# Optimization experiments

Measured on AMD Instinct MI355X. Metric: run time of the kernel, lower is better.

## Reference

```python
import jax, jax.numpy as jnp
import numpy as np

MIN_NORM = 1e-15
C = 1.0  # ball curvature from init kwargs
N, D, O = 16384, 512, 512


def _expmap0(u, c):
    sqrt_c = c ** 0.5
    u_norm = jnp.maximum(jnp.linalg.norm(u, axis=-1, keepdims=True), MIN_NORM)
    return jnp.tanh(sqrt_c * u_norm) * u / (sqrt_c * u_norm)


def setup_inputs() -> dict:
    key = jax.random.key(0)
    k1, k2, k3 = jax.random.split(key, 3)
    # scale inputs so they lie inside the unit Poincare ball (E||x|| ~ 0.45)
    x = jax.random.normal(k1, (N, D), jnp.float32) * 0.02
    point = _expmap0(jax.random.normal(k2, (O, D), jnp.float32) / 4, C)
    tangent = jax.random.normal(k3, (O, D), jnp.float32)
    tangent = tangent / jnp.maximum(jnp.linalg.norm(tangent, axis=-1, keepdims=True), MIN_NORM)  # sphere proj_
    scale = jnp.zeros((O,), jnp.float32)
    return {"x": x, "point": point, "tangent": tangent, "scale": scale}


def reference(x, point, tangent, scale):
    """Mobius dist2plane (signed) * exp(scale).

    Computes the reductions of diff = mobius_add(-p, x) analytically so the
    [N, O, D] broadcast intermediate of the original is never materialized.
    """
    c = C
    sqrt_c = c ** 0.5
    p, a = point, tangent
    p2 = jnp.sum(p * p, -1)                 # [O]  ||p||^2
    x2 = jnp.sum(x * x, -1)                 # [N]  ||x||^2
    xp = x @ p.T                             # [N,O] <x, p>
    xy = -xp                                 # <-p, x>
    # mobius_add(-p, x) = (A*(-p) + B*x) / Dn
    A = 1 + 2 * c * xy + c * x2[:, None]     # [N,O] coeff of -p
    B = 1 - c * p2                           # [O]   coeff of x
    Dn = jnp.maximum(1 + 2 * c * xy + (c * c) * p2[None, :] * x2[:, None], MIN_NORM)  # [N,O]
    pa = jnp.sum(p * a, -1)                  # [O]  <p, a>
    xa = x @ a.T                             # [N,O] <x, a>
    diff_norm2 = (A * A * p2[None, :] - 2 * A * B[None, :] * xp
                  + (B * B)[None, :] * x2[:, None]) / (Dn * Dn)
    diff_norm2 = jnp.maximum(diff_norm2, MIN_NORM)
    sc_diff_a = (-A * pa[None, :] + B[None, :] * xa) / Dn  # <diff, a>
    a_norm = jnp.maximum(jnp.linalg.norm(a, axis=-1), MIN_NORM)  # [O]
    num = 2 * sqrt_c * sc_diff_a
    denom = jnp.maximum((1 - c * diff_norm2) * a_norm[None, :], MIN_NORM)
    dist = jnp.arcsinh(num / denom) / sqrt_c  # [N,O]
    return dist * jnp.exp(scale)
```

## Files before the change

kernel.cpp:

```cpp
#include <hip/hip_runtime.h>
#include <hip/hip_bf16.h>

typedef float f32x4 __attribute__((ext_vector_type(4)));
typedef short short8_t __attribute__((ext_vector_type(8)));

__device__ __forceinline__ unsigned int cvt2(float lo, float hi) {
    unsigned int ul = __builtin_bit_cast(unsigned int, lo);
    unsigned int uh = __builtin_bit_cast(unsigned int, hi);
    ul += 0x7FFFu + ((ul >> 16) & 1u);
    uh += 0x7FFFu + ((uh >> 16) & 1u);
    return (ul >> 16) | (uh & 0xFFFF0000u);
}

__device__ __forceinline__ float sq4(f32x4 v, float acc) {
    acc = fmaf(v[0], v[0], acc); acc = fmaf(v[1], v[1], acc);
    acc = fmaf(v[2], v[2], acc); acc = fmaf(v[3], v[3], acc);
    return acc;
}

__device__ __forceinline__ float dot4(f32x4 a, f32x4 b, float acc) {
    acc = fmaf(a[0], b[0], acc); acc = fmaf(a[1], b[1], acc);
    acc = fmaf(a[2], b[2], acc); acc = fmaf(a[3], b[3], acc);
    return acc;
}

__device__ __forceinline__ short8_t pk8(f32x4 a, f32x4 b) {
    union { short8_t s; unsigned int u[4]; } w;
    w.u[0] = cvt2(a[0], a[1]); w.u[1] = cvt2(a[2], a[3]);
    w.u[2] = cvt2(b[0], b[1]); w.u[3] = cvt2(b[2], b[3]);
    return w.s;
}

__device__ __forceinline__ void gload16(const void* g, void* l) {
    __builtin_amdgcn_global_load_lds(
        (const __attribute__((address_space(1))) unsigned int*)g,
        (__attribute__((address_space(3))) unsigned int*)l, 16, 0, 0);
}

__global__ __launch_bounds__(256)
void prep_kernel(const float* __restrict__ X, const float* __restrict__ P,
                 const float* __restrict__ A, const float* __restrict__ S,
                 short* __restrict__ Xb, short* __restrict__ Pb, short* __restrict__ Ab,
                 float* __restrict__ x2a, float* __restrict__ paa, float* __restrict__ Ba,
                 float* __restrict__ rBana, float* __restrict__ esla, int N, int O)
{
    const int D = 512;
    const int w    = blockIdx.x * 4 + (threadIdx.x >> 6);
    const int lane = threadIdx.x & 63;
    if (w < N) {
        const float* row = X + (size_t)w * D + lane * 8;
        f32x4 u0 = *(const f32x4*)row;
        f32x4 u1 = *(const f32x4*)(row + 4);
        *(short8_t*)(Xb + (size_t)w * D + lane * 8) = pk8(u0, u1);
        float s = sq4(u1, sq4(u0, 0.f));
        #pragma unroll
        for (int m = 1; m < 64; m <<= 1) s += __shfl_xor(s, m, 64);
        if (lane == 0) x2a[w] = s;
    } else if (w < N + O) {
        const int col = w - N;
        const float* prow = P + (size_t)col * D + lane * 8;
        const float* arow = A + (size_t)col * D + lane * 8;
        f32x4 p0 = *(const f32x4*)prow, p1 = *(const f32x4*)(prow + 4);
        f32x4 a0 = *(const f32x4*)arow, a1 = *(const f32x4*)(arow + 4);
        *(short8_t*)(Pb + (size_t)col * D + lane * 8) = pk8(p0, p1);
        *(short8_t*)(Ab + (size_t)col * D + lane * 8) = pk8(a0, a1);
        float sp  = sq4(p1, sq4(p0, 0.f));
        float sa  = sq4(a1, sq4(a0, 0.f));
        float spa = dot4(p1, a1, dot4(p0, a0, 0.f));
        #pragma unroll
        for (int m = 1; m < 64; m <<= 1) {
            sp += __shfl_xor(sp, m, 64);
            sa += __shfl_xor(sa, m, 64);
            spa += __shfl_xor(spa, m, 64);
        }
        if (lane == 0) {
            float B  = 1.f - sp;
            float an = fmaxf(__builtin_amdgcn_sqrtf(sa), 1e-15f);
            paa[col]   = spa;
            Ba[col]    = B;
            rBana[col] = __builtin_amdgcn_rcpf(fmaxf(B * an, 1e-30f));
            esla[col]  = 0.69314718055994531f * expf(S[col]);
        }
    }
}

#define BM2 128
#define BN2 128
#define BK2 64

__global__ __launch_bounds__(256, 2)
void mobius_gemm_kernel(const short* __restrict__ Xb, const short* __restrict__ Pb,
                        const short* __restrict__ Ab,
                        const float* __restrict__ x2a, const float* __restrict__ paa,
                        const float* __restrict__ Ba, const float* __restrict__ rBana,
                        const float* __restrict__ esla,
                        float* __restrict__ out, int N, int O)
{
    const int D = 512;
    __shared__ __align__(16) char smem[3 * BM2 * BK2 * 2];
    char* xs = smem;
    char* ps = smem + 16384;
    char* as = smem + 32768;

    const int nwg = gridDim.x;
    const int q   = nwg >> 3;
    const int swz = (blockIdx.x & 7) * q + (blockIdx.x >> 3);
    const int ncol = O / BN2;
    const int brow = swz / ncol, bcol = swz % ncol;
    const int n0 = brow * BM2, o0 = bcol * BN2;

    const int tid = threadIdx.x, lane = tid & 63, wid = tid >> 6;
    const int wr = wid >> 1, wc = wid & 1;

    f32x4 accP[4][4], accA[4][4];
    #pragma unroll
    for (int m = 0; m < 4; m++)
        #pragma unroll
        for (int n = 0; n < 4; n++) { accP[m][n] = (f32x4)0.f; accA[m][n] = (f32x4)0.f; }

    const size_t Db = (size_t)D * 2;
    const char* Xc = (const char*)Xb;
    const char* Pc = (const char*)Pb;
    const char* Ac = (const char*)Ab;

    const int fr = lane & 15;
    const int fo = (lane >> 4) << 4;

    for (int ks = 0; ks < D / BK2; ++ks) {
        const size_t kb = (size_t)ks * (BK2 * 2);
        #pragma unroll
        for (int s = 0; s < 4; ++s) {
            int cl = s * 256 + tid, row = cl >> 3, ch = cl & 7;
            size_t rowoff = (size_t)row * Db + kb + (size_t)((ch ^ (row & 7)) << 4);
            gload16(Xc + (size_t)n0 * Db + rowoff, xs + cl * 16);
            gload16(Pc + (size_t)o0 * Db + rowoff, ps + cl * 16);
            gload16(Ac + (size_t)o0 * Db + rowoff, as + cl * 16);
        }
        __syncthreads();

        #pragma unroll
        for (int kk = 0; kk < 2; ++kk) {
            const int kx = (kk * 64 + fo) ^ ((lane & 7) << 4);
            short8_t af[4], bp[4], ba[4];
            #pragma unroll
            for (int m = 0; m < 4; m++)
                af[m] = *(const short8_t*)(xs + ((wr * 64 + m * 16 + fr) << 7) + kx);
            #pragma unroll
            for (int n = 0; n < 4; n++) {
                bp[n] = *(const short8_t*)(ps + ((wc * 64 + n * 16 + fr) << 7) + kx);
                ba[n] = *(const short8_t*)(as + ((wc * 64 + n * 16 + fr) << 7) + kx);
            }
            #pragma unroll
            for (int m = 0; m < 4; m++)
                #pragma unroll
                for (int n = 0; n < 4; n++) {
                    accP[m][n] = __builtin_amdgcn_mfma_f32_16x16x32_bf16(af[m], bp[n], accP[m][n], 0, 0, 0);
                    accA[m][n] = __builtin_amdgcn_mfma_f32_16x16x32_bf16(af[m], ba[n], accA[m][n], 0, 0, 0);
                }
        }
        __syncthreads();
    }

    const int cl_ = lane & 15, g = lane >> 4;
    float pac[4], Bc[4], rB[4], es[4];
    #pragma unroll
    for (int n = 0; n < 4; n++) {
        int col = o0 + wc * 64 + n * 16 + cl_;
        pac[n] = paa[col]; Bc[n] = Ba[col]; rB[n] = rBana[col]; es[n] = esla[col];
    }
    float* ob = (float*)smem;
    #pragma unroll
    for (int p = 0; p < 2; ++p) {
        if (wr == p) {
            #pragma unroll
            for (int m = 0; m < 4; m++) {
                #pragma unroll
                for (int r = 0; r < 4; r++) {
                    const int lrow = m * 16 + g * 4 + r;
                    const float x2  = x2a[n0 + p * 64 + lrow];
                    const float ap1 = 1.f + x2;
                    const float zs  = 2.f * __builtin_amdgcn_rcpf(fmaxf(1.f - x2, 1e-30f));
                    #pragma unroll
                    for (int n = 0; n < 4; n++) {
                        float xp = accP[m][n][r];
                        float xa = accA[m][n][r];
                        float Acf = ap1 - (xp + xp);
                        float num = fmaf(Bc[n], xa, -(Acf * pac[n]));
                        float z   = num * zs * rB[n];
                        float az  = fabsf(z);
                        float wv  = az + __builtin_amdgcn_sqrtf(fmaf(z, z, 1.f));
                        float l   = __builtin_amdgcn_logf(wv);
                        ob[lrow * 132 + wc * 64 + n * 16 + cl_] = copysignf(l, z) * es[n];
                    }
                }
            }
        }
        __syncthreads();
        #pragma unroll
        for (int s = 0; s < 8; ++s) {
            int row = s * 8 + (tid >> 5), c = (tid & 31) * 4;
            f32x4 v = *(const f32x4*)(ob + row * 132 + c);
            *(f32x4*)(out + (size_t)(n0 + p * 64 + row) * O + o0 + c) = v;
        }
        if (p == 0) __syncthreads();
    }
}

#define BM 128
#define BN 128
#define BK 64
#define PAD 8
#define LDT (BK + PAD)

__global__ __launch_bounds__(256, 2)
void mobius_d2p_kernel(const float* __restrict__ X, const float* __restrict__ P,
                       const float* __restrict__ A, const float* __restrict__ S,
                       float* __restrict__ out, int N, int O, int D)
{
    __shared__ short xs[BM][LDT];
    __shared__ short ps[BM][LDT];
    __shared__ short as_[BM][LDT];
    __shared__ float x2p[BM][2];
    __shared__ float p2p[BM][2];
    __shared__ float pap[BM][2];
    __shared__ float a2p[BM][2];

    const int nwg = gridDim.x;
    int swz = blockIdx.x;
    if ((nwg & 7) == 0) {
        int q = nwg >> 3;
        swz = (blockIdx.x & 7) * q + (blockIdx.x >> 3);
    }
    const int ncol = O / BN;
    const int brow = swz / ncol;
    const int bcol = swz % ncol;
    const int n0 = brow * BM;
    const int o0 = bcol * BN;

    const int tid  = threadIdx.x;
    const int lane = tid & 63;
    const int wid  = tid >> 6;
    const int wr   = wid >> 1;
    const int wc   = wid & 1;

    const int srow = tid >> 1;
    const int sseg = (tid & 1) * 32;

    const float* xg = X + (size_t)(n0 + srow) * D + sseg;
    const float* pg = P + (size_t)(o0 + srow) * D + sseg;
    const float* ag = A + (size_t)(o0 + srow) * D + sseg;

    float accx2 = 0.f, accp2 = 0.f, accpa = 0.f, acca2 = 0.f;

    f32x4 accP[4][4], accA[4][4];
    #pragma unroll
    for (int i = 0; i < 4; i++)
        #pragma unroll
        for (int j = 0; j < 4; j++) { accP[i][j] = (f32x4)0.f; accA[i][j] = (f32x4)0.f; }

    const int frow_a = wr * 64 + (lane & 15);
    const int frow_b = wc * 64 + (lane & 15);
    const int fk     = (lane >> 4) * 8;

    const int nk = D / BK;
    for (int ks = 0; ks < nk; ++ks) {
        const float* xr = xg + ks * BK;
        const float* pr = pg + ks * BK;
        const float* ar = ag + ks * BK;

        #pragma unroll
        for (int j = 0; j < 4; j++) {
            f32x4 u0 = *(const f32x4*)(xr + j * 8);
            f32x4 u1 = *(const f32x4*)(xr + j * 8 + 4);
            accx2 = sq4(u0, accx2); accx2 = sq4(u1, accx2);
            *(short8_t*)&xs[srow][sseg + j * 8] = pk8(u0, u1);
        }
        #pragma unroll
        for (int j = 0; j < 4; j++) {
            f32x4 u0 = *(const f32x4*)(pr + j * 8);
            f32x4 u1 = *(const f32x4*)(pr + j * 8 + 4);
            f32x4 v0 = *(const f32x4*)(ar + j * 8);
            f32x4 v1 = *(const f32x4*)(ar + j * 8 + 4);
            accp2 = sq4(u0, accp2); accp2 = sq4(u1, accp2);
            acca2 = sq4(v0, acca2); acca2 = sq4(v1, acca2);
            accpa = dot4(u0, v0, accpa); accpa = dot4(u1, v1, accpa);
            *(short8_t*)&ps[srow][sseg + j * 8] = pk8(u0, u1);
            *(short8_t*)&as_[srow][sseg + j * 8] = pk8(v0, v1);
        }
        __syncthreads();

        #pragma unroll
        for (int kk = 0; kk < 2; ++kk) {
            const int kof = kk * 32 + fk;
            short8_t af[4], bp[4], ba[4];
            #pragma unroll
            for (int m = 0; m < 4; m++) af[m] = *(const short8_t*)&xs[frow_a + m * 16][kof];
            #pragma unroll
            for (int n = 0; n < 4; n++) {
                bp[n] = *(const short8_t*)&ps[frow_b + n * 16][kof];
                ba[n] = *(const short8_t*)&as_[frow_b + n * 16][kof];
            }
            #pragma unroll
            for (int m = 0; m < 4; m++)
                #pragma unroll
                for (int n = 0; n < 4; n++) {
                    accP[m][n] = __builtin_amdgcn_mfma_f32_16x16x32_bf16(af[m], bp[n], accP[m][n], 0, 0, 0);
                    accA[m][n] = __builtin_amdgcn_mfma_f32_16x16x32_bf16(af[m], ba[n], accA[m][n], 0, 0, 0);
                }
        }
        __syncthreads();
    }

    x2p[srow][tid & 1] = accx2;
    p2p[srow][tid & 1] = accp2;
    pap[srow][tid & 1] = accpa;
    a2p[srow][tid & 1] = acca2;
    __syncthreads();

    const int cl = lane & 15;
    const int g  = lane >> 4;

    float pac[4], Bcv[4], rBan[4], esl[4];
    #pragma unroll
    for (int n = 0; n < 4; n++) {
        int col = wc * 64 + n * 16 + cl;
        float p2 = p2p[col][0] + p2p[col][1];
        float pa = pap[col][0] + pap[col][1];
        float a2 = a2p[col][0] + a2p[col][1];
        float B  = 1.f - p2;
        float an = fmaxf(__builtin_amdgcn_sqrtf(a2), 1e-15f);
        pac[n] = pa; Bcv[n] = B;
        rBan[n] = __builtin_amdgcn_rcpf(fmaxf(B * an, 1e-30f));
        esl[n]  = 0.69314718055994531f * expf(S[o0 + col]);
    }
    float x2r[16];
    #pragma unroll
    for (int m = 0; m < 4; m++)
        #pragma unroll
        for (int r = 0; r < 4; r++) {
            int row = wr * 64 + m * 16 + g * 4 + r;
            x2r[m * 4 + r] = x2p[row][0] + x2p[row][1];
        }

    #pragma unroll
    for (int m = 0; m < 4; m++) {
        #pragma unroll
        for (int r = 0; r < 4; r++) {
            const int row = wr * 64 + m * 16 + g * 4 + r;
            const float x2  = x2r[m * 4 + r];
            const float ap1 = 1.f + x2;
            const float zs  = 2.f * __builtin_amdgcn_rcpf(fmaxf(1.f - x2, 1e-30f));
            float* orow = out + (size_t)(n0 + row) * O + o0 + wc * 64 + cl;
            #pragma unroll
            for (int n = 0; n < 4; n++) {
                float xp = accP[m][n][r];
                float xa = accA[m][n][r];
                float Ac = ap1 - (xp + xp);
                float num = fmaf(Bcv[n], xa, -(Ac * pac[n]));
                float z   = num * zs * rBan[n];
                float az = fabsf(z);
                float w  = az + __builtin_amdgcn_sqrtf(fmaf(z, z, 1.f));
                float l  = __builtin_amdgcn_logf(w);
                orow[n * 16] = copysignf(l, z) * esl[n];
            }
        }
    }
}

extern "C" void kernel_launch(void* const* d_in, const int* in_sizes, int n_in,
                              void* d_out, int out_size, void* d_ws, size_t ws_size,
                              hipStream_t stream) {
    const float* X = (const float*)d_in[0];
    const float* P = (const float*)d_in[1];
    const float* A = (const float*)d_in[2];
    const float* S = (const float*)d_in[3];
    float* out = (float*)d_out;

    const int O = in_sizes[3];
    const int D = in_sizes[1] / O;
    const int N = in_sizes[0] / D;

    size_t offP  = (size_t)N * D * 2;
    size_t offA  = offP + (size_t)O * D * 2;
    size_t offx2 = offA + (size_t)O * D * 2;
    size_t offpa = offx2 + (size_t)N * 4;
    size_t offB  = offpa + (size_t)O * 4;
    size_t offrB = offB + (size_t)O * 4;
    size_t offes = offrB + (size_t)O * 4;
    size_t need  = offes + (size_t)O * 4;

    const bool fast = (ws_size >= need) && D == 512 &&
                      (N % BM2 == 0) && (O % BN2 == 0) &&
                      (((N / BM2) * (O / BN2)) % 8 == 0) && ((N + O) % 4 == 0);

    if (fast) {
        char* ws = (char*)d_ws;
        short* Xb = (short*)ws;
        short* Pb = (short*)(ws + offP);
        short* Ab = (short*)(ws + offA);
        float* x2a = (float*)(ws + offx2);
        float* paa = (float*)(ws + offpa);
        float* Ba  = (float*)(ws + offB);
        float* rBa = (float*)(ws + offrB);
        float* esl = (float*)(ws + offes);

        prep_kernel<<<dim3((N + O) / 4), dim3(256), 0, stream>>>(
            X, P, A, S, Xb, Pb, Ab, x2a, paa, Ba, rBa, esl, N, O);
        mobius_gemm_kernel<<<dim3((N / BM2) * (O / BN2)), dim3(256), 0, stream>>>(
            Xb, Pb, Ab, x2a, paa, Ba, rBa, esl, out, N, O);
    } else {
        const int nwg = (N / BM) * (O / BN);
        mobius_d2p_kernel<<<dim3(nwg), dim3(256), 0, stream>>>(X, P, A, S, out, N, O, D);
    }
}
```

Measured before the change: 111.0 us.

## Double-buffer LDS tiles and enlarge GEMM row tile to 256 with 512 threads

Global-to-LDS staging of the X, P and A tiles for the next K step is now issued before the MFMA work on the current step. The buffers alternate in 128KB of dynamic shared memory, which overlaps load latency with compute and drops one barrier per iteration. The block tile grows from 128 to 256 rows with 8 waves, so each P/A tile is reused across more rows. In exchange LDS use allows only one block per CU, and the grid shrinks to about one block per CU, which can hurt latency hiding and leave the load unbalanced.

```diff
diff --git a/kernel.cpp b/kernel.cpp
--- a/kernel.cpp
+++ b/kernel.cpp
@@ -84,11 +84,31 @@
     }
 }
 
-#define BM2 128
+#define BM2 256
 #define BN2 128
 #define BK2 64
-
-__global__ __launch_bounds__(256, 2)
+#define BUFB 65536
+
+__device__ __forceinline__ void stage_tiles2(const char* Xc, const char* Pc, const char* Ac,
+                                             char* buf, int n0, int o0, int ks, int tid,
+                                             size_t Db) {
+    const size_t kb = (size_t)ks * (BK2 * 2);
+    #pragma unroll
+    for (int s = 0; s < 4; ++s) {
+        int cl = s * 512 + tid, row = cl >> 3, ch = cl & 7;
+        gload16(Xc + (size_t)(n0 + row) * Db + kb + (size_t)((ch ^ (row & 7)) << 4),
+                buf + cl * 16);
+    }
+    #pragma unroll
+    for (int s = 0; s < 2; ++s) {
+        int cl = s * 512 + tid, row = cl >> 3, ch = cl & 7;
+        size_t go = (size_t)(o0 + row) * Db + kb + (size_t)((ch ^ (row & 7)) << 4);
+        gload16(Pc + go, buf + 32768 + cl * 16);
+        gload16(Ac + go, buf + 49152 + cl * 16);
+    }
+}
+
+__global__ __launch_bounds__(512, 2)
 void mobius_gemm_kernel(const short* __restrict__ Xb, const short* __restrict__ Pb,
                         const short* __restrict__ Ab,
                         const float* __restrict__ x2a, const float* __restrict__ paa,
@@ -97,10 +117,7 @@
                         float* __restrict__ out, int N, int O)
 {
     const int D = 512;
-    __shared__ __align__(16) char smem[3 * BM2 * BK2 * 2];
-    char* xs = smem;
-    char* ps = smem + 16384;
-    char* as = smem + 32768;
+    extern __shared__ __align__(16) char smem[];
 
     const int nwg = gridDim.x;
     const int q   = nwg >> 3;
@@ -126,17 +143,18 @@
     const int fr = lane & 15;
     const int fo = (lane >> 4) << 4;
 
-    for (int ks = 0; ks < D / BK2; ++ks) {
-        const size_t kb = (size_t)ks * (BK2 * 2);
-        #pragma unroll
-        for (int s = 0; s < 4; ++s) {
-            int cl = s * 256 + tid, row = cl >> 3, ch = cl & 7;
-            size_t rowoff = (size_t)row * Db + kb + (size_t)((ch ^ (row & 7)) << 4);
-            gload16(Xc + (size_t)n0 * Db + rowoff, xs + cl * 16);
-            gload16(Pc + (size_t)o0 * Db + rowoff, ps + cl * 16);
-            gload16(Ac + (size_t)o0 * Db + rowoff, as + cl * 16);
-        }
-        __syncthreads();
+    stage_tiles2(Xc, Pc, Ac, smem, n0, o0, 0, tid, Db);
+    __syncthreads();
+
+    int cur = 0;
+    const int NK = D / BK2;
+    for (int ks = 0; ks < NK; ++ks) {
+        if (ks + 1 < NK)
+            stage_tiles2(Xc, Pc, Ac, smem + (cur ^ 1) * BUFB, n0, o0, ks + 1, tid, Db);
+
+        const char* xs = smem + cur * BUFB;
+        const char* ps = xs + 32768;
+        const char* as = xs + 49152;
 
         #pragma unroll
         for (int kk = 0; kk < 2; ++kk) {
@@ -159,6 +177,7 @@
                 }
         }
         __syncthreads();
+        cur ^= 1;
     }
 
     const int cl_ = lane & 15, g = lane >> 4;
@@ -171,13 +190,13 @@
     float* ob = (float*)smem;
     #pragma unroll
     for (int p = 0; p < 2; ++p) {
-        if (wr == p) {
+        if ((wr >> 1) == p) {
             #pragma unroll
             for (int m = 0; m < 4; m++) {
                 #pragma unroll
                 for (int r = 0; r < 4; r++) {
-                    const int lrow = m * 16 + g * 4 + r;
-                    const float x2  = x2a[n0 + p * 64 + lrow];
+                    const int lrow = (wr & 1) * 64 + m * 16 + g * 4 + r;
+                    const float x2  = x2a[n0 + p * 128 + lrow];
                     const float ap1 = 1.f + x2;
                     const float zs  = 2.f * __builtin_amdgcn_rcpf(fmaxf(1.f - x2, 1e-30f));
                     #pragma unroll
@@ -198,9 +217,9 @@
         __syncthreads();
         #pragma unroll
         for (int s = 0; s < 8; ++s) {
-            int row = s * 8 + (tid >> 5), c = (tid & 31) * 4;
+            int row = s * 16 + (tid >> 5), c = (tid & 31) * 4;
             f32x4 v = *(const f32x4*)(ob + row * 132 + c);
-            *(f32x4*)(out + (size_t)(n0 + p * 64 + row) * O + o0 + c) = v;
+            *(f32x4*)(out + (size_t)(n0 + p * 128 + row) * O + o0 + c) = v;
         }
         if (p == 0) __syncthreads();
     }
@@ -389,9 +408,16 @@
     size_t offes = offrB + (size_t)O * 4;
     size_t need  = offes + (size_t)O * 4;
 
-    const bool fast = (ws_size >= need) && D == 512 &&
-                      (N % BM2 == 0) && (O % BN2 == 0) &&
-                      (((N / BM2) * (O / BN2)) % 8 == 0) && ((N + O) % 4 == 0);
+    bool fast = (ws_size >= need) && D == 512 &&
+                (N % BM2 == 0) && (O % BN2 == 0) &&
+                (((N / BM2) * (O / BN2)) % 8 == 0) && ((N + O) % 4 == 0);
+
+    if (fast) {
+        hipError_t e = hipFuncSetAttribute(
+            (const void*)mobius_gemm_kernel,
+            hipFuncAttributeMaxDynamicSharedMemorySize, 2 * BUFB);
+        if (e != hipSuccess) fast = false;
+    }
 
     if (fast) {
         char* ws = (char*)d_ws;
@@ -406,7 +432,7 @@
 
         prep_kernel<<<dim3((N + O) / 4), dim3(256), 0, stream>>>(
             X, P, A, S, Xb, Pb, Ab, x2a, paa, Ba, rBa, esl, N, O);
-        mobius_gemm_kernel<<<dim3((N / BM2) * (O / BN2)), dim3(256), 0, stream>>>(
+        mobius_gemm_kernel<<<dim3((N / BM2) * (O / BN2)), dim3(512), 2 * BUFB, stream>>>(
             Xb, Pb, Ab, x2a, paa, Ba, rBa, esl, out, N, O);
     } else {
         const int nwg = (N / BM) * (O / BN);
```

Measured after the change: 111.7 us. No clear change (+0.6%).

## Pre-swizzle bf16 operands into MFMA fragment order and load directly from global

Applied to the files above, without the earlier changes.

The prep kernel now writes X, P and A in a layout that matches the MFMA 16x32 fragment order, so each lane's 16-byte operand is contiguous. The GEMM kernel drops the LDS staging, the global-to-LDS loads and the per-step barriers, and has each wave read its fragments straight from global/L2. This removes LDS traffic and synchronisation, but each wave now fetches its operands separately with no sharing through LDS, so it relies on L2 reuse and on latency hiding from the unrolled loop.

```diff
diff --git a/kernel.cpp b/kernel.cpp
--- a/kernel.cpp
+++ b/kernel.cpp
@@ -31,16 +31,10 @@
     return w.s;
 }
 
-__device__ __forceinline__ void gload16(const void* g, void* l) {
-    __builtin_amdgcn_global_load_lds(
-        (const __attribute__((address_space(1))) unsigned int*)g,
-        (__attribute__((address_space(3))) unsigned int*)l, 16, 0, 0);
-}
-
 __global__ __launch_bounds__(256)
 void prep_kernel(const float* __restrict__ X, const float* __restrict__ P,
                  const float* __restrict__ A, const float* __restrict__ S,
-                 short* __restrict__ Xb, short* __restrict__ Pb, short* __restrict__ Ab,
+                 short* __restrict__ Xf, short* __restrict__ Pf, short* __restrict__ Af,
                  float* __restrict__ x2a, float* __restrict__ paa, float* __restrict__ Ba,
                  float* __restrict__ rBana, float* __restrict__ esla, int N, int O)
 {
@@ -51,7 +45,8 @@
         const float* row = X + (size_t)w * D + lane * 8;
         f32x4 u0 = *(const f32x4*)row;
         f32x4 u1 = *(const f32x4*)(row + 4);
-        *(short8_t*)(Xb + (size_t)w * D + lane * 8) = pk8(u0, u1);
+        size_t sl = ((size_t)(w >> 4) * 16 + (lane >> 2)) * 64 + (size_t)(lane & 3) * 16 + (w & 15);
+        *(short8_t*)(Xf + sl * 8) = pk8(u0, u1);
         float s = sq4(u1, sq4(u0, 0.f));
         #pragma unroll
         for (int m = 1; m < 64; m <<= 1) s += __shfl_xor(s, m, 64);
@@ -62,8 +57,9 @@
         const float* arow = A + (size_t)col * D + lane * 8;
         f32x4 p0 = *(const f32x4*)prow, p1 = *(const f32x4*)(prow + 4);
         f32x4 a0 = *(const f32x4*)arow, a1 = *(const f32x4*)(arow + 4);
-        *(short8_t*)(Pb + (size_t)col * D + lane * 8) = pk8(p0, p1);
-        *(short8_t*)(Ab + (size_t)col * D + lane * 8) = pk8(a0, a1);
+        size_t sl = ((size_t)(col >> 4) * 16 + (lane >> 2)) * 64 + (size_t)(lane & 3) * 16 + (col & 15);
+        *(short8_t*)(Pf + sl * 8) = pk8(p0, p1);
+        *(short8_t*)(Af + sl * 8) = pk8(a0, a1);
         float sp  = sq4(p1, sq4(p0, 0.f));
         float sa  = sq4(a1, sq4(a0, 0.f));
         float spa = dot4(p1, a1, dot4(p0, a0, 0.f));
@@ -86,7 +82,6 @@
 
 #define BM2 128
 #define BN2 128
-#define BK2 64
 
 __global__ __launch_bounds__(256, 2)
 void mobius_gemm_kernel(const short* __restrict__ Xb, const short* __restrict__ Pb,
@@ -96,11 +91,7 @@
                         const float* __restrict__ esla,
                         float* __restrict__ out, int N, int O)
 {
-    const int D = 512;
-    __shared__ __align__(16) char smem[3 * BM2 * BK2 * 2];
-    char* xs = smem;
-    char* ps = smem + 16384;
-    char* as = smem + 32768;
+    __shared__ float ob[64 * 132];
 
     const int nwg = gridDim.x;
     const int q   = nwg >> 3;
@@ -118,47 +109,31 @@
         #pragma unroll
         for (int n = 0; n < 4; n++) { accP[m][n] = (f32x4)0.f; accA[m][n] = (f32x4)0.f; }
 
-    const size_t Db = (size_t)D * 2;
-    const char* Xc = (const char*)Xb;
-    const char* Pc = (const char*)Pb;
-    const char* Ac = (const char*)Ab;
-
-    const int fr = lane & 15;
-    const int fo = (lane >> 4) << 4;
-
-    for (int ks = 0; ks < D / BK2; ++ks) {
-        const size_t kb = (size_t)ks * (BK2 * 2);
-        #pragma unroll
-        for (int s = 0; s < 4; ++s) {
-            int cl = s * 256 + tid, row = cl >> 3, ch = cl & 7;
-            size_t rowoff = (size_t)row * Db + kb + (size_t)((ch ^ (row & 7)) << 4);
-            gload16(Xc + (size_t)n0 * Db + rowoff, xs + cl * 16);
-            gload16(Pc + (size_t)o0 * Db + rowoff, ps + cl * 16);
-            gload16(Ac + (size_t)o0 * Db + rowoff, as + cl * 16);
-        }
-        __syncthreads();
-
-        #pragma unroll
-        for (int kk = 0; kk < 2; ++kk) {
-            const int kx = (kk * 64 + fo) ^ ((lane & 7) << 4);
-            short8_t af[4], bp[4], ba[4];
-            #pragma unroll
-            for (int m = 0; m < 4; m++)
-                af[m] = *(const short8_t*)(xs + ((wr * 64 + m * 16 + fr) << 7) + kx);
+    const short8_t* Xf = (const short8_t*)Xb;
+    const short8_t* Pf = (const short8_t*)Pb;
+    const short8_t* Af = (const short8_t*)Ab;
+
+    const size_t abase = ((size_t)((n0 >> 4) + wr * 4) * 16) * 64 + lane;
+    const size_t bbase = ((size_t)((o0 >> 4) + wc * 4) * 16) * 64 + lane;
+
+    #pragma unroll 4
+    for (int st = 0; st < 16; ++st) {
+        const size_t ko = (size_t)st * 64;
+        short8_t af[4], bp[4], ba[4];
+        #pragma unroll
+        for (int m = 0; m < 4; m++) af[m] = Xf[abase + (size_t)m * 1024 + ko];
+        #pragma unroll
+        for (int n = 0; n < 4; n++) {
+            bp[n] = Pf[bbase + (size_t)n * 1024 + ko];
+            ba[n] = Af[bbase + (size_t)n * 1024 + ko];
+        }
+        #pragma unroll
+        for (int m = 0; m < 4; m++)
             #pragma unroll
             for (int n = 0; n < 4; n++) {
-                bp[n] = *(const short8_t*)(ps + ((wc * 64 + n * 16 + fr) << 7) + kx);
-                ba[n] = *(const short8_t*)(as + ((wc * 64 + n * 16 + fr) << 7) + kx);
+                accP[m][n] = __builtin_amdgcn_mfma_f32_16x16x32_bf16(af[m], bp[n], accP[m][n], 0, 0, 0);
+                accA[m][n] = __builtin_amdgcn_mfma_f32_16x16x32_bf16(af[m], ba[n], accA[m][n], 0, 0, 0);
             }
-            #pragma unroll
-            for (int m = 0; m < 4; m++)
-                #pragma unroll
-                for (int n = 0; n < 4; n++) {
-                    accP[m][n] = __builtin_amdgcn_mfma_f32_16x16x32_bf16(af[m], bp[n], accP[m][n], 0, 0, 0);
-                    accA[m][n] = __builtin_amdgcn_mfma_f32_16x16x32_bf16(af[m], ba[n], accA[m][n], 0, 0, 0);
-                }
-        }
-        __syncthreads();
     }
 
     const int cl_ = lane & 15, g = lane >> 4;
@@ -168,7 +143,6 @@
         int col = o0 + wc * 64 + n * 16 + cl_;
         pac[n] = paa[col]; Bc[n] = Ba[col]; rB[n] = rBana[col]; es[n] = esla[col];
     }
-    float* ob = (float*)smem;
     #pragma unroll
     for (int p = 0; p < 2; ++p) {
         if (wr == p) {
@@ -390,14 +364,14 @@
     size_t need  = offes + (size_t)O * 4;
 
     const bool fast = (ws_size >= need) && D == 512 &&
-                      (N % BM2 == 0) && (O % BN2 == 0) &&
+                      (N % BM2 == 0) && (O % BN2 == 0) && (N % 16 == 0) && (O % 16 == 0) &&
                       (((N / BM2) * (O / BN2)) % 8 == 0) && ((N + O) % 4 == 0);
 
     if (fast) {
         char* ws = (char*)d_ws;
-        short* Xb = (short*)ws;
-        short* Pb = (short*)(ws + offP);
-        short* Ab = (short*)(ws + offA);
+        short* Xf = (short*)ws;
+        short* Pf = (short*)(ws + offP);
+        short* Af = (short*)(ws + offA);
         float* x2a = (float*)(ws + offx2);
         float* paa = (float*)(ws + offpa);
         float* Ba  = (float*)(ws + offB);
@@ -405,9 +379,9 @@
         float* esl = (float*)(ws + offes);
 
         prep_kernel<<<dim3((N + O) / 4), dim3(256), 0, stream>>>(
-            X, P, A, S, Xb, Pb, Ab, x2a, paa, Ba, rBa, esl, N, O);
+            X, P, A, S, Xf, Pf, Af, x2a, paa, Ba, rBa, esl, N, O);
         mobius_gemm_kernel<<<dim3((N / BM2) * (O / BN2)), dim3(256), 0, stream>>>(
-            Xb, Pb, Ab, x2a, paa, Ba, rBa, esl, out, N, O);
+            Xf, Pf, Af, x2a, paa, Ba, rBa, esl, out, N, O);
     } else {
         const int nwg = (N / BM) * (O / BN);
         mobius_d2p_kernel<<<dim3(nwg), dim3(256), 0, stream>>>(X, P, A, S, out, N, O, D);
```

Measured after the change: 115.7 us. 4.2% more time.
